# Kernel tuning notes

Measured on AMD Instinct MI355X. Metric: run time of the kernel, lower is better.

## Reference

```python
import jax, jax.numpy as jnp
import numpy as np

N_NODES = 100000
N_EDGES = 1600000
IN_C, HID_C, OUT_C = 128, 256, 128


def setup_inputs() -> dict:
    key = jax.random.key(0)
    ks = jax.random.split(key, 6)
    x = jax.random.normal(ks[0], (N_NODES, IN_C), dtype=jnp.float32)
    edge_index = jax.random.randint(ks[1], (2, N_EDGES), 0, N_NODES, dtype=jnp.int64)
    s = 0.05
    W1a = jax.random.normal(ks[2], (IN_C, HID_C), dtype=jnp.float32) * s
    b1a = jnp.zeros((HID_C,), dtype=jnp.float32)
    W2a = jax.random.normal(ks[3], (HID_C, HID_C), dtype=jnp.float32) * s
    b2a = jnp.zeros((HID_C,), dtype=jnp.float32)
    W1b = jax.random.normal(ks[4], (HID_C, HID_C), dtype=jnp.float32) * s
    b1b = jnp.zeros((HID_C,), dtype=jnp.float32)
    W2b = jax.random.normal(ks[5], (HID_C, OUT_C), dtype=jnp.float32) * s
    b2b = jnp.zeros((OUT_C,), dtype=jnp.float32)
    return {"x": x, "edge_index": edge_index, "W1a": W1a, "b1a": b1a,
            "W2a": W2a, "b2a": b2a, "W1b": W1b, "b1b": b1b,
            "W2b": W2b, "b2b": b2b}


def _gin_conv(x, src, dst, W1, b1, W2, b2):
    # GINConv (eps=0): nn( x + sum_{j in N(i)} x_j )
    agg = jax.ops.segment_sum(x[src], dst, num_segments=N_NODES)  # [N, d]
    h = x + agg
    h = jnp.maximum(h @ W1 + b1, 0.0)
    return h @ W2 + b2


def reference(x, edge_index, W1a, b1a, W2a, b2a, W1b, b1b, W2b, b2b):
    src, dst = edge_index[0], edge_index[1]
    h = jnp.maximum(_gin_conv(x, src, dst, W1a, b1a, W2a, b2a), 0.0)  # relu(conv1)
    # dropout is identity in eval mode
    out = _gin_conv(h, src, dst, W1b, b1b, W2b, b2b)  # conv2
    return out
```

## Files before the change

### kernel.cpp

```cpp
#include <hip/hip_runtime.h>


#define N_NODES 100000
#define N_EDGES 1600000
#define NBUCK 13

typedef unsigned short ushort_t;
typedef short bf16x8 __attribute__((ext_vector_type(8)));
typedef float floatx4 __attribute__((ext_vector_type(4)));

static __device__ __forceinline__ ushort_t f2bf(float f) {
    unsigned u = __float_as_uint(f);
    u = (u + 0x7FFFu + ((u >> 16) & 1u)) >> 16;
    return (ushort_t)u;
}
static __device__ __forceinline__ unsigned pack2bf(float lo, float hi) {
    return (unsigned)f2bf(lo) | ((unsigned)f2bf(hi) << 16);
}
static __device__ __forceinline__ void addu4(float* acc, const uint4 v) {
    const unsigned w0 = v.x, w1 = v.y, w2 = v.z, w3 = v.w;
    acc[0] += __uint_as_float(w0 << 16);
    acc[1] += __uint_as_float(w0 & 0xFFFF0000u);
    acc[2] += __uint_as_float(w1 << 16);
    acc[3] += __uint_as_float(w1 & 0xFFFF0000u);
    acc[4] += __uint_as_float(w2 << 16);
    acc[5] += __uint_as_float(w2 & 0xFFFF0000u);
    acc[6] += __uint_as_float(w3 << 16);
    acc[7] += __uint_as_float(w3 & 0xFFFF0000u);
}

#define GLOAD_LDS16(g, l)                                                     \
    __builtin_amdgcn_global_load_lds(                                         \
        (const __attribute__((address_space(1))) void*)(g),                   \
        (__attribute__((address_space(3))) void*)(l), 16, 0, 0)

#define NX8 (N_NODES * 128 / 8)
__global__ __launch_bounds__(256) void cvt_fused_kernel(
    const float* __restrict__ X, ushort_t* __restrict__ Xb,
    const float* __restrict__ W1a, const float* __restrict__ W2a,
    const float* __restrict__ W1b, const float* __restrict__ W2b,
    ushort_t* __restrict__ wt1a, ushort_t* __restrict__ wt2a,
    ushort_t* __restrict__ wt1b, ushort_t* __restrict__ wt2b) {
    int i = blockIdx.x * 256 + threadIdx.x;
    if (i < NX8) {
        const float4 a = ((const float4*)X)[2 * i];
        const float4 b = ((const float4*)X)[2 * i + 1];
        uint4 r;
        r.x = pack2bf(a.x, a.y);
        r.y = pack2bf(a.z, a.w);
        r.z = pack2bf(b.x, b.y);
        r.w = pack2bf(b.z, b.w);
        ((uint4*)Xb)[i] = r;
        return;
    }
    i -= NX8;
    if (i < 32768) {
        int k = i >> 8, n = i & 255;
        wt1a[n * 128 + k] = f2bf(W1a[i]);
    } else if (i < 98304) {
        int j = i - 32768, k = j >> 8, n = j & 255;
        wt2a[n * 256 + k] = f2bf(W2a[j]);
    } else if (i < 163840) {
        int j = i - 98304, k = j >> 8, n = j & 255;
        wt1b[n * 256 + k] = f2bf(W1b[j]);
    } else if (i < 196608) {
        int j = i - 163840, k = j >> 7, n = j & 127;
        wt2b[n * 256 + k] = f2bf(W2b[j]);
    }
}

__global__ __launch_bounds__(256) void hist_kernel(const int* __restrict__ src,
                                                   const int* __restrict__ dst,
                                                   int* __restrict__ deg, int nE) {
    for (int e = blockIdx.x * 256 + threadIdx.x; e < nE; e += gridDim.x * 256) {
        int d = dst[e];
        int s = src[e];
        if ((unsigned)d < (unsigned)N_NODES && (unsigned)s < (unsigned)N_NODES)
            atomicAdd(&deg[d], 1);
    }
}

__global__ __launch_bounds__(256) void fill_kernel(const int* __restrict__ src,
                                                   const int* __restrict__ dst,
                                                   int* __restrict__ cursor,
                                                   int* __restrict__ csr_src, int nE) {
    const int bucket = blockIdx.y;
    for (int e = blockIdx.x * 256 + threadIdx.x; e < nE; e += gridDim.x * 256) {
        int d = dst[e];
        int s = src[e];
        if ((unsigned)d < (unsigned)N_NODES && (unsigned)s < (unsigned)N_NODES &&
            (d >> 13) == bucket) {
            int pos = atomicAdd(&cursor[d], 1);
            csr_src[pos] = s;
        }
    }
}

__global__ __launch_bounds__(256) void scan1_kernel(const int* __restrict__ deg,
                                                    int* __restrict__ bsum, int n) {
    __shared__ int l[256];
    int b = blockIdx.x, t = threadIdx.x;
    int base = b * 1024 + t * 4;
    int s = 0;
#pragma unroll
    for (int k = 0; k < 4; ++k) {
        int i = base + k;
        if (i < n) s += deg[i];
    }
    l[t] = s;
    __syncthreads();
    for (int off = 128; off > 0; off >>= 1) {
        if (t < off) l[t] += l[t + off];
        __syncthreads();
    }
    if (t == 0) bsum[b] = l[0];
}

__global__ __launch_bounds__(128) void scan2_kernel(const int* __restrict__ bsum,
                                                    int* __restrict__ boff, int nb) {
    __shared__ int l[128];
    int t = threadIdx.x;
    int v = (t < nb) ? bsum[t] : 0;
    l[t] = v;
    __syncthreads();
    for (int off = 1; off < 128; off <<= 1) {
        int add = (t >= off) ? l[t - off] : 0;
        __syncthreads();
        l[t] += add;
        __syncthreads();
    }
    if (t < nb) boff[t] = l[t] - v;
}

__global__ __launch_bounds__(256) void scan3_kernel(const int* __restrict__ deg,
                                                    const int* __restrict__ boff,
                                                    int* __restrict__ row_ptr,
                                                    int* __restrict__ cursor, int n) {
    __shared__ int l[256];
    int b = blockIdx.x, t = threadIdx.x;
    int base = b * 1024 + t * 4;
    int d[4];
    int s = 0;
#pragma unroll
    for (int k = 0; k < 4; ++k) {
        int i = base + k;
        d[k] = (i < n) ? deg[i] : 0;
        s += d[k];
    }
    l[t] = s;
    __syncthreads();
    for (int off = 1; off < 256; off <<= 1) {
        int add = (t >= off) ? l[t - off] : 0;
        __syncthreads();
        l[t] += add;
        __syncthreads();
    }
    int run = boff[b] + l[t] - s;
#pragma unroll
    for (int k = 0; k < 4; ++k) {
        int i = base + k;
        if (i < n) {
            row_ptr[i] = run;
            cursor[i] = run;
        }
        run += d[k];
    }
}

template <int C, int U>
__global__ __launch_bounds__(256) void agg_gather_kernel(
    const ushort_t* __restrict__ X, ushort_t* __restrict__ T,
    const int* __restrict__ row_ptr, const int* __restrict__ deg,
    const int* __restrict__ csr_src, const ushort_t* __restrict__ zrow, int nN) {
    constexpr int G = C / 8;
    constexpr int NPW = 64 / G;
    constexpr int B = U * NPW;
    const int lane = threadIdx.x & 63;
    const int wid = threadIdx.x >> 6;
    const int node = blockIdx.x * 4 + wid;
    if (node >= nN) return;
    const int sub = lane / G;
    const int coff = (lane % G) * 8;

    float acc[8];
#pragma unroll
    for (int k = 0; k < 8; ++k) acc[k] = 0.f;

    const int base = row_ptr[node];
    const int dg = deg[node];
    for (int j0 = 0; j0 < dg; j0 += 64) {
        int cnt = dg - j0;
        if (cnt > 64) cnt = 64;
        int nidx = (lane < cnt) ? csr_src[base + j0 + lane] : 0;
        if ((unsigned)nidx >= (unsigned)N_NODES) nidx = 0;
        for (int j = 0; j < cnt; j += B) {
            uint4 v[U];
#pragma unroll
            for (int u = 0; u < U; ++u) {
                int jj = j + u * NPW + sub;
                bool ok = jj < cnt;
                int idx = __shfl(nidx, ok ? jj : 0);
                const ushort_t* p = ok ? (X + (size_t)idx * C) : zrow;
                v[u] = *(const uint4*)(p + coff);
            }
#pragma unroll
            for (int u = 0; u < U; ++u) addu4(acc, v[u]);
        }
    }
    if (sub == 0) {
        uint4 v = *(const uint4*)(X + (size_t)node * C + coff);
        addu4(acc, v);
    }
#pragma unroll
    for (int off = G; off < 64; off <<= 1)
#pragma unroll
        for (int k = 0; k < 8; ++k) acc[k] += __shfl_xor(acc[k], off);

    if (lane < G) {
        uint4 r;
        r.x = pack2bf(acc[0], acc[1]);
        r.y = pack2bf(acc[2], acc[3]);
        r.z = pack2bf(acc[4], acc[5]);
        r.w = pack2bf(acc[6], acc[7]);
        *(uint4*)(T + (size_t)node * C + coff) = r;
    }
}

template <int K1, int N2, bool RELU2, typename OT>
__global__ __launch_bounds__(256, 3) void mlp_kernel(
    const ushort_t* __restrict__ A, const ushort_t* __restrict__ Wt1,
    const float* __restrict__ b1, const ushort_t* __restrict__ Wt2,
    const float* __restrict__ b2, OT* __restrict__ C, int M) {
    constexpr int N1 = 256, BM = 64, BK = 32;
    constexpr int NPW2 = N2 / 4;
    constexpr int RN2 = NPW2 / 16;
    __shared__ ushort_t As[BM * BK];
    __shared__ ushort_t Bs[N1 * BK];
    __shared__ ushort_t U[BM * N1];

    const int lane = threadIdx.x & 63;
    const int wid = threadIdx.x >> 6;
    const int l15 = lane & 15;
    const int q = lane >> 4;
    const int srow = lane >> 2;
    const int scol = (lane & 3) * 8;
    const int bm = blockIdx.x * BM;

    floatx4 acc[4][4];
#pragma unroll
    for (int mi = 0; mi < 4; ++mi)
#pragma unroll
        for (int ni = 0; ni < 4; ++ni) {
            floatx4 z = {0.f, 0.f, 0.f, 0.f};
            acc[mi][ni] = z;
        }

    for (int kt = 0; kt < K1; kt += BK) {
        {
            const int gr = bm + wid * 16 + srow;
            if (gr < M)
                GLOAD_LDS16(A + (size_t)gr * K1 + kt + scol, &As[(wid * 16) * BK]);
        }
#pragma unroll
        for (int u = 0; u < 4; ++u) {
            const int row = wid * 64 + u * 16;
            GLOAD_LDS16(Wt1 + (size_t)(row + srow) * K1 + kt + scol, &Bs[row * BK]);
        }
        __syncthreads();
        bf16x8 av[4], bv[4];
#pragma unroll
        for (int mi = 0; mi < 4; ++mi)
            av[mi] = *(const bf16x8*)&Bs[(wid * 64 + mi * 16 + l15) * BK + q * 8];
#pragma unroll
        for (int ni = 0; ni < 4; ++ni)
            bv[ni] = *(const bf16x8*)&As[(ni * 16 + l15) * BK + q * 8];
#pragma unroll
        for (int mi = 0; mi < 4; ++mi)
#pragma unroll
            for (int ni = 0; ni < 4; ++ni)
                acc[mi][ni] = __builtin_amdgcn_mfma_f32_16x16x32_bf16(
                    av[mi], bv[ni], acc[mi][ni], 0, 0, 0);
        __syncthreads();
    }

#pragma unroll
    for (int mi = 0; mi < 4; ++mi) {
        const int h0 = wid * 64 + mi * 16 + q * 4;
        const float4 b4 = *(const float4*)&b1[h0];
#pragma unroll
        for (int ni = 0; ni < 4; ++ni) {
            const int node = ni * 16 + l15;
            float v0 = acc[mi][ni][0] + b4.x; v0 = v0 > 0.f ? v0 : 0.f;
            float v1 = acc[mi][ni][1] + b4.y; v1 = v1 > 0.f ? v1 : 0.f;
            float v2 = acc[mi][ni][2] + b4.z; v2 = v2 > 0.f ? v2 : 0.f;
            float v3 = acc[mi][ni][3] + b4.w; v3 = v3 > 0.f ? v3 : 0.f;
            uint2 w;
            w.x = pack2bf(v0, v1);
            w.y = pack2bf(v2, v3);
            int byte = node * (N1 * 2) + h0 * 2;
            byte ^= (node & 7) << 4;
            *(uint2*)((char*)U + byte) = w;
        }
    }
    __syncthreads();

#pragma unroll
    for (int mi = 0; mi < 4; ++mi)
#pragma unroll
        for (int ni = 0; ni < 4; ++ni) {
            floatx4 z = {0.f, 0.f, 0.f, 0.f};
            acc[mi][ni] = z;
        }

    for (int kt = 0; kt < N1; kt += BK) {
#pragma unroll
        for (int u = 0; u < RN2; ++u) {
            const int row = wid * NPW2 + u * 16;
            GLOAD_LDS16(Wt2 + (size_t)(row + srow) * N1 + kt + scol, &Bs[row * BK]);
        }
        __syncthreads();
        bf16x8 av[4], bv[RN2];
#pragma unroll
        for (int mi = 0; mi < 4; ++mi) {
            const int node = mi * 16 + l15;
            const int byte =
                (node * (N1 * 2) + kt * 2 + q * 16) ^ ((node & 7) << 4);
            av[mi] = *(const bf16x8*)((const char*)U + byte);
        }
#pragma unroll
        for (int ni = 0; ni < RN2; ++ni)
            bv[ni] = *(const bf16x8*)&Bs[(wid * NPW2 + ni * 16 + l15) * BK + q * 8];
#pragma unroll
        for (int mi = 0; mi < 4; ++mi)
#pragma unroll
            for (int ni = 0; ni < RN2; ++ni)
                acc[mi][ni] = __builtin_amdgcn_mfma_f32_16x16x32_bf16(
                    av[mi], bv[ni], acc[mi][ni], 0, 0, 0);
        __syncthreads();
    }

    float bval[RN2];
#pragma unroll
    for (int ni = 0; ni < RN2; ++ni) bval[ni] = b2[wid * NPW2 + ni * 16 + l15];
#pragma unroll
    for (int mi = 0; mi < 4; ++mi) {
#pragma unroll
        for (int r = 0; r < 4; ++r) {
            const int row = bm + mi * 16 + q * 4 + r;
            if (row < M) {
#pragma unroll
                for (int ni = 0; ni < RN2; ++ni) {
                    const int col = wid * NPW2 + ni * 16 + l15;
                    float v = acc[mi][ni][r] + bval[ni];
                    if (RELU2) v = v > 0.f ? v : 0.f;
                    if constexpr (sizeof(OT) == 2)
                        C[(size_t)row * N2 + col] = f2bf(v);
                    else
                        C[(size_t)row * N2 + col] = v;
                }
            }
        }
    }
}

extern "C" void kernel_launch(void* const* d_in, const int* in_sizes, int n_in,
                              void* d_out, int out_size, void* d_ws, size_t ws_size,
                              hipStream_t stream) {
    const float* x   = (const float*)d_in[0];
    const int*   ei  = (const int*)d_in[1];
    const float* W1a = (const float*)d_in[2];
    const float* b1a = (const float*)d_in[3];
    const float* W2a = (const float*)d_in[4];
    const float* b2a = (const float*)d_in[5];
    const float* W1b = (const float*)d_in[6];
    const float* b1b = (const float*)d_in[7];
    const float* W2b = (const float*)d_in[8];
    const float* b2b = (const float*)d_in[9];
    const int* src = ei;
    const int* dst = ei + N_EDGES;
    float* out = (float*)d_out;

    char* base = (char*)d_ws;
    size_t o = 0;
    ushort_t* wt1a = (ushort_t*)(base + o); o += 128 * 256 * 2;
    ushort_t* wt2a = (ushort_t*)(base + o); o += 256 * 256 * 2;
    ushort_t* wt1b = (ushort_t*)(base + o); o += 256 * 256 * 2;
    ushort_t* wt2b = (ushort_t*)(base + o); o += 256 * 128 * 2;
    o = (o + 255) & ~(size_t)255;
    ushort_t* zrow = (ushort_t*)(base + o); o += 512;
    int* deg     = (int*)(base + o); o += (size_t)N_NODES * 4;
    int* row_ptr = (int*)(base + o); o += (size_t)N_NODES * 4;
    int* cursor  = (int*)(base + o); o += (size_t)N_NODES * 4;
    int* bsum    = (int*)(base + o); o += 128 * 4;
    int* boff    = (int*)(base + o); o += 128 * 4;
    o = (o + 255) & ~(size_t)255;
    int* csr_src = (int*)(base + o); o += (size_t)N_EDGES * 4;
    o = (o + 255) & ~(size_t)255;
    ushort_t* t1   = (ushort_t*)(base + o); o += (size_t)N_NODES * 128 * 2;
    ushort_t* tbig = (ushort_t*)(base + o); o += (size_t)N_NODES * 256 * 2;
    o += 128 * 1024;
    (void)ws_size; (void)o; (void)in_sizes; (void)n_in; (void)out_size;

    ushort_t* inter = (ushort_t*)d_out;
    ushort_t* xb    = (ushort_t*)d_out;

    cvt_fused_kernel<<<(NX8 + 196608 + 255) / 256, 256, 0, stream>>>(
        x, xb, W1a, W2a, W1b, W2b, wt1a, wt2a, wt1b, wt2b);

    const int NB = (N_NODES + 1023) / 1024;
    hipMemsetAsync(zrow, 0, 512 + (size_t)N_NODES * 4, stream);
    hist_kernel<<<2048, 256, 0, stream>>>(src, dst, deg, N_EDGES);
    scan1_kernel<<<NB, 256, 0, stream>>>(deg, bsum, N_NODES);
    scan2_kernel<<<1, 128, 0, stream>>>(bsum, boff, NB);
    scan3_kernel<<<NB, 256, 0, stream>>>(deg, boff, row_ptr, cursor, N_NODES);
    fill_kernel<<<dim3(1024, NBUCK), 256, 0, stream>>>(src, dst, cursor, csr_src,
                                                       N_EDGES);

    const int ga = (N_NODES + 3) / 4;
    const int gf = (N_NODES + 63) / 64;

    agg_gather_kernel<128, 4><<<ga, 256, 0, stream>>>(xb, t1, row_ptr, deg,
                                                      csr_src, zrow, N_NODES);
    mlp_kernel<128, 256, true, ushort_t><<<gf, 256, 0, stream>>>(
        t1, wt1a, b1a, wt2a, b2a, inter, N_NODES);

    agg_gather_kernel<256, 8><<<ga, 256, 0, stream>>>(inter, tbig, row_ptr,
                                                      deg, csr_src, zrow, N_NODES);
    mlp_kernel<256, 128, false, float><<<gf, 256, 0, stream>>>(
        tbig, wt1b, b1b, wt2b, b2b, out, N_NODES);
}
```

Baseline: 532.4 us.

## Double-buffer LDS tiles in fused MLP kernel to overlap loads with MFMA

Splits the As and Bs shared tiles in the fused two-layer MLP kernel into two buffers each. The next K-tile's global-to-LDS load is issued before the MFMAs on the current tile, removing one barrier per iteration. The first second-layer weight tile is also prefetched while the first-layer epilogue writes the hidden activations. The larger LDS footprint forces launch bounds down from 3 to 2 blocks per CU, trading occupancy for load/compute overlap.

```diff
diff --git a/kernel.cpp b/kernel.cpp
--- a/kernel.cpp
+++ b/kernel.cpp
@@ -227,15 +227,17 @@
 }
 
 template <int K1, int N2, bool RELU2, typename OT>
-__global__ __launch_bounds__(256, 3) void mlp_kernel(
+__global__ __launch_bounds__(256, 2) void mlp_kernel(
     const ushort_t* __restrict__ A, const ushort_t* __restrict__ Wt1,
     const float* __restrict__ b1, const ushort_t* __restrict__ Wt2,
     const float* __restrict__ b2, OT* __restrict__ C, int M) {
     constexpr int N1 = 256, BM = 64, BK = 32;
     constexpr int NPW2 = N2 / 4;
     constexpr int RN2 = NPW2 / 16;
-    __shared__ ushort_t As[BM * BK];
-    __shared__ ushort_t Bs[N1 * BK];
+    constexpr int NT1 = K1 / BK;
+    constexpr int NT2 = N1 / BK;
+    __shared__ ushort_t As[2][BM * BK];
+    __shared__ ushort_t Bs[2][N1 * BK];
     __shared__ ushort_t U[BM * N1];
 
     const int lane = threadIdx.x & 63;
@@ -246,6 +248,26 @@
     const int scol = (lane & 3) * 8;
     const int bm = blockIdx.x * BM;
 
+    auto stage1 = [&](int bf, int kt) {
+        const int gr = bm + wid * 16 + srow;
+        if (gr < M)
+            GLOAD_LDS16(A + (size_t)gr * K1 + kt + scol, &As[bf][(wid * 16) * BK]);
+#pragma unroll
+        for (int u = 0; u < 4; ++u) {
+            const int row = wid * 64 + u * 16;
+            GLOAD_LDS16(Wt1 + (size_t)(row + srow) * K1 + kt + scol,
+                        &Bs[bf][row * BK]);
+        }
+    };
+    auto stage2 = [&](int bf, int kt) {
+#pragma unroll
+        for (int u = 0; u < RN2; ++u) {
+            const int row = wid * NPW2 + u * 16;
+            GLOAD_LDS16(Wt2 + (size_t)(row + srow) * N1 + kt + scol,
+                        &Bs[bf][row * BK]);
+        }
+    };
+
     floatx4 acc[4][4];
 #pragma unroll
     for (int mi = 0; mi < 4; ++mi)
@@ -255,25 +277,18 @@
             acc[mi][ni] = z;
         }
 
-    for (int kt = 0; kt < K1; kt += BK) {
-        {
-            const int gr = bm + wid * 16 + srow;
-            if (gr < M)
-                GLOAD_LDS16(A + (size_t)gr * K1 + kt + scol, &As[(wid * 16) * BK]);
-        }
-#pragma unroll
-        for (int u = 0; u < 4; ++u) {
-            const int row = wid * 64 + u * 16;
-            GLOAD_LDS16(Wt1 + (size_t)(row + srow) * K1 + kt + scol, &Bs[row * BK]);
-        }
-        __syncthreads();
+    stage1(0, 0);
+    __syncthreads();
+    for (int t = 0; t < NT1; ++t) {
+        if (t + 1 < NT1) stage1((t + 1) & 1, (t + 1) * BK);
+        const int cb = t & 1;
         bf16x8 av[4], bv[4];
 #pragma unroll
         for (int mi = 0; mi < 4; ++mi)
-            av[mi] = *(const bf16x8*)&Bs[(wid * 64 + mi * 16 + l15) * BK + q * 8];
+            av[mi] = *(const bf16x8*)&Bs[cb][(wid * 64 + mi * 16 + l15) * BK + q * 8];
 #pragma unroll
         for (int ni = 0; ni < 4; ++ni)
-            bv[ni] = *(const bf16x8*)&As[(ni * 16 + l15) * BK + q * 8];
+            bv[ni] = *(const bf16x8*)&As[cb][(ni * 16 + l15) * BK + q * 8];
 #pragma unroll
         for (int mi = 0; mi < 4; ++mi)
 #pragma unroll
@@ -282,6 +297,8 @@
                     av[mi], bv[ni], acc[mi][ni], 0, 0, 0);
         __syncthreads();
     }
+
+    stage2(0, 0);
 
 #pragma unroll
     for (int mi = 0; mi < 4; ++mi) {
@@ -312,13 +329,10 @@
             acc[mi][ni] = z;
         }
 
-    for (int kt = 0; kt < N1; kt += BK) {
-#pragma unroll
-        for (int u = 0; u < RN2; ++u) {
-            const int row = wid * NPW2 + u * 16;
-            GLOAD_LDS16(Wt2 + (size_t)(row + srow) * N1 + kt + scol, &Bs[row * BK]);
-        }
-        __syncthreads();
+    for (int t = 0; t < NT2; ++t) {
+        if (t + 1 < NT2) stage2((t + 1) & 1, (t + 1) * BK);
+        const int cb = t & 1;
+        const int kt = t * BK;
         bf16x8 av[4], bv[RN2];
 #pragma unroll
         for (int mi = 0; mi < 4; ++mi) {
@@ -329,7 +343,7 @@
         }
 #pragma unroll
         for (int ni = 0; ni < RN2; ++ni)
-            bv[ni] = *(const bf16x8*)&Bs[(wid * NPW2 + ni * 16 + l15) * BK + q * 8];
+            bv[ni] = *(const bf16x8*)&Bs[cb][(wid * NPW2 + ni * 16 + l15) * BK + q * 8];
 #pragma unroll
         for (int mi = 0; mi < 4; ++mi)
 #pragma unroll
```

Result: slower. 544.5 us (+2.3%).

## Fuse degree histogram into conversion kernel, halve fill buckets, pack accumulators

Applied to the files above, without the earlier changes.

Merges the edge degree histogram into the bf16 conversion launch as extra blocks, which removes one kernel launch and lets the two independent jobs overlap. The CSR fill pass now uses 7 destination buckets of 16384 nodes instead of 13 of 8192, so the edge list is re-read fewer times, at the cost of a larger atomic/write footprint per bucket. The gather accumulators become float2 vectors, which may let the compiler emit packed FP32 adds. The memset is moved ahead of the fused kernel so deg is zeroed before the histogram atomics run.

```diff
diff --git a/kernel.cpp b/kernel.cpp
--- a/kernel.cpp
+++ b/kernel.cpp
@@ -3,11 +3,12 @@
 
 #define N_NODES 100000
 #define N_EDGES 1600000
-#define NBUCK 13
+#define NBUCK 7
 
 typedef unsigned short ushort_t;
 typedef short bf16x8 __attribute__((ext_vector_type(8)));
 typedef float floatx4 __attribute__((ext_vector_type(4)));
+typedef float floatx2 __attribute__((ext_vector_type(2)));
 
 static __device__ __forceinline__ ushort_t f2bf(float f) {
     unsigned u = __float_as_uint(f);
@@ -17,16 +18,16 @@
 static __device__ __forceinline__ unsigned pack2bf(float lo, float hi) {
     return (unsigned)f2bf(lo) | ((unsigned)f2bf(hi) << 16);
 }
-static __device__ __forceinline__ void addu4(float* acc, const uint4 v) {
+static __device__ __forceinline__ void addu4(floatx2* acc, const uint4 v) {
     const unsigned w0 = v.x, w1 = v.y, w2 = v.z, w3 = v.w;
-    acc[0] += __uint_as_float(w0 << 16);
-    acc[1] += __uint_as_float(w0 & 0xFFFF0000u);
-    acc[2] += __uint_as_float(w1 << 16);
-    acc[3] += __uint_as_float(w1 & 0xFFFF0000u);
-    acc[4] += __uint_as_float(w2 << 16);
-    acc[5] += __uint_as_float(w2 & 0xFFFF0000u);
-    acc[6] += __uint_as_float(w3 << 16);
-    acc[7] += __uint_as_float(w3 & 0xFFFF0000u);
+    floatx2 a0 = {__uint_as_float(w0 << 16), __uint_as_float(w0 & 0xFFFF0000u)};
+    floatx2 a1 = {__uint_as_float(w1 << 16), __uint_as_float(w1 & 0xFFFF0000u)};
+    floatx2 a2 = {__uint_as_float(w2 << 16), __uint_as_float(w2 & 0xFFFF0000u)};
+    floatx2 a3 = {__uint_as_float(w3 << 16), __uint_as_float(w3 & 0xFFFF0000u)};
+    acc[0] += a0;
+    acc[1] += a1;
+    acc[2] += a2;
+    acc[3] += a3;
 }
 
 #define GLOAD_LDS16(g, l)                                                     \
@@ -35,12 +36,16 @@
         (__attribute__((address_space(3))) void*)(l), 16, 0, 0)
 
 #define NX8 (N_NODES * 128 / 8)
+#define CVT_TOTAL (NX8 + 196608)
+#define HIST_THREADS (2048 * 256)
 __global__ __launch_bounds__(256) void cvt_fused_kernel(
     const float* __restrict__ X, ushort_t* __restrict__ Xb,
     const float* __restrict__ W1a, const float* __restrict__ W2a,
     const float* __restrict__ W1b, const float* __restrict__ W2b,
     ushort_t* __restrict__ wt1a, ushort_t* __restrict__ wt2a,
-    ushort_t* __restrict__ wt1b, ushort_t* __restrict__ wt2b) {
+    ushort_t* __restrict__ wt1b, ushort_t* __restrict__ wt2b,
+    const int* __restrict__ src, const int* __restrict__ dst,
+    int* __restrict__ deg, int nE) {
     int i = blockIdx.x * 256 + threadIdx.x;
     if (i < NX8) {
         const float4 a = ((const float4*)X)[2 * i];
@@ -53,26 +58,24 @@
         ((uint4*)Xb)[i] = r;
         return;
     }
-    i -= NX8;
-    if (i < 32768) {
-        int k = i >> 8, n = i & 255;
-        wt1a[n * 128 + k] = f2bf(W1a[i]);
-    } else if (i < 98304) {
-        int j = i - 32768, k = j >> 8, n = j & 255;
-        wt2a[n * 256 + k] = f2bf(W2a[j]);
-    } else if (i < 163840) {
-        int j = i - 98304, k = j >> 8, n = j & 255;
-        wt1b[n * 256 + k] = f2bf(W1b[j]);
-    } else if (i < 196608) {
-        int j = i - 163840, k = j >> 7, n = j & 127;
-        wt2b[n * 256 + k] = f2bf(W2b[j]);
-    }
-}
-
-__global__ __launch_bounds__(256) void hist_kernel(const int* __restrict__ src,
-                                                   const int* __restrict__ dst,
-                                                   int* __restrict__ deg, int nE) {
-    for (int e = blockIdx.x * 256 + threadIdx.x; e < nE; e += gridDim.x * 256) {
+    if (i < CVT_TOTAL) {
+        i -= NX8;
+        if (i < 32768) {
+            int k = i >> 8, n = i & 255;
+            wt1a[n * 128 + k] = f2bf(W1a[i]);
+        } else if (i < 98304) {
+            int j = i - 32768, k = j >> 8, n = j & 255;
+            wt2a[n * 256 + k] = f2bf(W2a[j]);
+        } else if (i < 163840) {
+            int j = i - 98304, k = j >> 8, n = j & 255;
+            wt1b[n * 256 + k] = f2bf(W1b[j]);
+        } else {
+            int j = i - 163840, k = j >> 7, n = j & 127;
+            wt2b[n * 256 + k] = f2bf(W2b[j]);
+        }
+        return;
+    }
+    for (int e = i - CVT_TOTAL; e < nE; e += HIST_THREADS) {
         int d = dst[e];
         int s = src[e];
         if ((unsigned)d < (unsigned)N_NODES && (unsigned)s < (unsigned)N_NODES)
@@ -89,7 +92,7 @@
         int d = dst[e];
         int s = src[e];
         if ((unsigned)d < (unsigned)N_NODES && (unsigned)s < (unsigned)N_NODES &&
-            (d >> 13) == bucket) {
+            (d >> 14) == bucket) {
             int pos = atomicAdd(&cursor[d], 1);
             csr_src[pos] = s;
         }
@@ -182,9 +185,12 @@
     const int sub = lane / G;
     const int coff = (lane % G) * 8;
 
-    float acc[8];
-#pragma unroll
-    for (int k = 0; k < 8; ++k) acc[k] = 0.f;
+    floatx2 acc[4];
+#pragma unroll
+    for (int k = 0; k < 4; ++k) {
+        floatx2 z = {0.f, 0.f};
+        acc[k] = z;
+    }
 
     const int base = row_ptr[node];
     const int dg = deg[node];
@@ -214,14 +220,17 @@
 #pragma unroll
     for (int off = G; off < 64; off <<= 1)
 #pragma unroll
-        for (int k = 0; k < 8; ++k) acc[k] += __shfl_xor(acc[k], off);
+        for (int k = 0; k < 4; ++k) {
+            acc[k][0] += __shfl_xor(acc[k][0], off);
+            acc[k][1] += __shfl_xor(acc[k][1], off);
+        }
 
     if (lane < G) {
         uint4 r;
-        r.x = pack2bf(acc[0], acc[1]);
-        r.y = pack2bf(acc[2], acc[3]);
-        r.z = pack2bf(acc[4], acc[5]);
-        r.w = pack2bf(acc[6], acc[7]);
+        r.x = pack2bf(acc[0][0], acc[0][1]);
+        r.y = pack2bf(acc[1][0], acc[1][1]);
+        r.z = pack2bf(acc[2][0], acc[2][1]);
+        r.w = pack2bf(acc[3][0], acc[3][1]);
         *(uint4*)(T + (size_t)node * C + coff) = r;
     }
 }
@@ -404,12 +413,12 @@
     ushort_t* inter = (ushort_t*)d_out;
     ushort_t* xb    = (ushort_t*)d_out;
 
-    cvt_fused_kernel<<<(NX8 + 196608 + 255) / 256, 256, 0, stream>>>(
-        x, xb, W1a, W2a, W1b, W2b, wt1a, wt2a, wt1b, wt2b);
+    hipMemsetAsync(zrow, 0, 512 + (size_t)N_NODES * 4, stream);
+
+    cvt_fused_kernel<<<CVT_TOTAL / 256 + 2048, 256, 0, stream>>>(
+        x, xb, W1a, W2a, W1b, W2b, wt1a, wt2a, wt1b, wt2b, src, dst, deg, N_EDGES);
 
     const int NB = (N_NODES + 1023) / 1024;
-    hipMemsetAsync(zrow, 0, 512 + (size_t)N_NODES * 4, stream);
-    hist_kernel<<<2048, 256, 0, stream>>>(src, dst, deg, N_EDGES);
     scan1_kernel<<<NB, 256, 0, stream>>>(deg, bsum, N_NODES);
     scan2_kernel<<<1, 128, 0, stream>>>(bsum, boff, NB);
     scan3_kernel<<<NB, 256, 0, stream>>>(deg, boff, row_ptr, cursor, N_NODES);
```

Result: no change. 538.9 us (+1.2%).

## Fuse histogram into convert kernel, merge scan passes, widen MLP to 8 waves

Applied to the files above, without the earlier changes.

The degree histogram now runs inside the fused conversion kernel as extra blocks, and the separate block-offset scan kernel is removed: each scan3 block reduces the preceding block sums itself. This drops two launches. The MLP kernel moves to 512 threads (8 waves), with each wave taking half the hidden and output columns. That halves per-wave accumulator registers and aims for more waves in flight, but adds idle waves during A-tile loads and more work per barrier.

```diff
diff --git a/kernel.cpp b/kernel.cpp
--- a/kernel.cpp
+++ b/kernel.cpp
@@ -35,12 +35,16 @@
         (__attribute__((address_space(3))) void*)(l), 16, 0, 0)
 
 #define NX8 (N_NODES * 128 / 8)
+#define CVT_TOTAL (NX8 + 196608)
+#define HIST_THREADS (2048 * 256)
 __global__ __launch_bounds__(256) void cvt_fused_kernel(
     const float* __restrict__ X, ushort_t* __restrict__ Xb,
     const float* __restrict__ W1a, const float* __restrict__ W2a,
     const float* __restrict__ W1b, const float* __restrict__ W2b,
     ushort_t* __restrict__ wt1a, ushort_t* __restrict__ wt2a,
-    ushort_t* __restrict__ wt1b, ushort_t* __restrict__ wt2b) {
+    ushort_t* __restrict__ wt1b, ushort_t* __restrict__ wt2b,
+    const int* __restrict__ src, const int* __restrict__ dst,
+    int* __restrict__ deg, int nE) {
     int i = blockIdx.x * 256 + threadIdx.x;
     if (i < NX8) {
         const float4 a = ((const float4*)X)[2 * i];
@@ -53,26 +57,24 @@
         ((uint4*)Xb)[i] = r;
         return;
     }
-    i -= NX8;
-    if (i < 32768) {
-        int k = i >> 8, n = i & 255;
-        wt1a[n * 128 + k] = f2bf(W1a[i]);
-    } else if (i < 98304) {
-        int j = i - 32768, k = j >> 8, n = j & 255;
-        wt2a[n * 256 + k] = f2bf(W2a[j]);
-    } else if (i < 163840) {
-        int j = i - 98304, k = j >> 8, n = j & 255;
-        wt1b[n * 256 + k] = f2bf(W1b[j]);
-    } else if (i < 196608) {
-        int j = i - 163840, k = j >> 7, n = j & 127;
-        wt2b[n * 256 + k] = f2bf(W2b[j]);
-    }
-}
-
-__global__ __launch_bounds__(256) void hist_kernel(const int* __restrict__ src,
-                                                   const int* __restrict__ dst,
-                                                   int* __restrict__ deg, int nE) {
-    for (int e = blockIdx.x * 256 + threadIdx.x; e < nE; e += gridDim.x * 256) {
+    if (i < CVT_TOTAL) {
+        i -= NX8;
+        if (i < 32768) {
+            int k = i >> 8, n = i & 255;
+            wt1a[n * 128 + k] = f2bf(W1a[i]);
+        } else if (i < 98304) {
+            int j = i - 32768, k = j >> 8, n = j & 255;
+            wt2a[n * 256 + k] = f2bf(W2a[j]);
+        } else if (i < 163840) {
+            int j = i - 98304, k = j >> 8, n = j & 255;
+            wt1b[n * 256 + k] = f2bf(W1b[j]);
+        } else {
+            int j = i - 163840, k = j >> 7, n = j & 127;
+            wt2b[n * 256 + k] = f2bf(W2b[j]);
+        }
+        return;
+    }
+    for (int e = i - CVT_TOTAL; e < nE; e += HIST_THREADS) {
         int d = dst[e];
         int s = src[e];
         if ((unsigned)d < (unsigned)N_NODES && (unsigned)s < (unsigned)N_NODES)
@@ -116,28 +118,22 @@
     if (t == 0) bsum[b] = l[0];
 }
 
-__global__ __launch_bounds__(128) void scan2_kernel(const int* __restrict__ bsum,
-                                                    int* __restrict__ boff, int nb) {
-    __shared__ int l[128];
-    int t = threadIdx.x;
-    int v = (t < nb) ? bsum[t] : 0;
-    l[t] = v;
+__global__ __launch_bounds__(256) void scan3_kernel(const int* __restrict__ deg,
+                                                    const int* __restrict__ bsum,
+                                                    int* __restrict__ row_ptr,
+                                                    int* __restrict__ cursor,
+                                                    int n, int nb) {
+    __shared__ int l[256];
+    __shared__ int boffs;
+    int b = blockIdx.x, t = threadIdx.x;
+    l[t] = (t < b && t < nb) ? bsum[t] : 0;
     __syncthreads();
-    for (int off = 1; off < 128; off <<= 1) {
-        int add = (t >= off) ? l[t - off] : 0;
-        __syncthreads();
-        l[t] += add;
-        __syncthreads();
-    }
-    if (t < nb) boff[t] = l[t] - v;
-}
-
-__global__ __launch_bounds__(256) void scan3_kernel(const int* __restrict__ deg,
-                                                    const int* __restrict__ boff,
-                                                    int* __restrict__ row_ptr,
-                                                    int* __restrict__ cursor, int n) {
-    __shared__ int l[256];
-    int b = blockIdx.x, t = threadIdx.x;
+    for (int off = 128; off > 0; off >>= 1) {
+        if (t < off) l[t] += l[t + off];
+        __syncthreads();
+    }
+    if (t == 0) boffs = l[0];
+    __syncthreads();
     int base = b * 1024 + t * 4;
     int d[4];
     int s = 0;
@@ -155,7 +151,7 @@
         l[t] += add;
         __syncthreads();
     }
-    int run = boff[b] + l[t] - s;
+    int run = boffs + l[t] - s;
 #pragma unroll
     for (int k = 0; k < 4; ++k) {
         int i = base + k;
@@ -227,12 +223,12 @@
 }
 
 template <int K1, int N2, bool RELU2, typename OT>
-__global__ __launch_bounds__(256, 3) void mlp_kernel(
+__global__ __launch_bounds__(512, 4) void mlp_kernel(
     const ushort_t* __restrict__ A, const ushort_t* __restrict__ Wt1,
     const float* __restrict__ b1, const ushort_t* __restrict__ Wt2,
     const float* __restrict__ b2, OT* __restrict__ C, int M) {
     constexpr int N1 = 256, BM = 64, BK = 32;
-    constexpr int NPW2 = N2 / 4;
+    constexpr int NPW2 = N2 / 8;
     constexpr int RN2 = NPW2 / 16;
     __shared__ ushort_t As[BM * BK];
     __shared__ ushort_t Bs[N1 * BK];
@@ -246,54 +242,54 @@
     const int scol = (lane & 3) * 8;
     const int bm = blockIdx.x * BM;
 
-    floatx4 acc[4][4];
-#pragma unroll
-    for (int mi = 0; mi < 4; ++mi)
+    floatx4 acc1[2][4];
+#pragma unroll
+    for (int mi = 0; mi < 2; ++mi)
 #pragma unroll
         for (int ni = 0; ni < 4; ++ni) {
             floatx4 z = {0.f, 0.f, 0.f, 0.f};
-            acc[mi][ni] = z;
+            acc1[mi][ni] = z;
         }
 
     for (int kt = 0; kt < K1; kt += BK) {
-        {
+        if (wid < 4) {
             const int gr = bm + wid * 16 + srow;
             if (gr < M)
                 GLOAD_LDS16(A + (size_t)gr * K1 + kt + scol, &As[(wid * 16) * BK]);
         }
 #pragma unroll
-        for (int u = 0; u < 4; ++u) {
-            const int row = wid * 64 + u * 16;
+        for (int u = 0; u < 2; ++u) {
+            const int row = wid * 32 + u * 16;
             GLOAD_LDS16(Wt1 + (size_t)(row + srow) * K1 + kt + scol, &Bs[row * BK]);
         }
         __syncthreads();
-        bf16x8 av[4], bv[4];
-#pragma unroll
-        for (int mi = 0; mi < 4; ++mi)
-            av[mi] = *(const bf16x8*)&Bs[(wid * 64 + mi * 16 + l15) * BK + q * 8];
+        bf16x8 av[2], bv[4];
+#pragma unroll
+        for (int mi = 0; mi < 2; ++mi)
+            av[mi] = *(const bf16x8*)&Bs[(wid * 32 + mi * 16 + l15) * BK + q * 8];
 #pragma unroll
         for (int ni = 0; ni < 4; ++ni)
             bv[ni] = *(const bf16x8*)&As[(ni * 16 + l15) * BK + q * 8];
 #pragma unroll
-        for (int mi = 0; mi < 4; ++mi)
+        for (int mi = 0; mi < 2; ++mi)
 #pragma unroll
             for (int ni = 0; ni < 4; ++ni)
-                acc[mi][ni] = __builtin_amdgcn_mfma_f32_16x16x32_bf16(
-                    av[mi], bv[ni], acc[mi][ni], 0, 0, 0);
-        __syncthreads();
-    }
-
-#pragma unroll
-    for (int mi = 0; mi < 4; ++mi) {
-        const int h0 = wid * 64 + mi * 16 + q * 4;
+                acc1[mi][ni] = __builtin_amdgcn_mfma_f32_16x16x32_bf16(
+                    av[mi], bv[ni], acc1[mi][ni], 0, 0, 0);
+        __syncthreads();
+    }
+
+#pragma unroll
+    for (int mi = 0; mi < 2; ++mi) {
+        const int h0 = wid * 32 + mi * 16 + q * 4;
         const float4 b4 = *(const float4*)&b1[h0];
 #pragma unroll
         for (int ni = 0; ni < 4; ++ni) {
             const int node = ni * 16 + l15;
-            float v0 = acc[mi][ni][0] + b4.x; v0 = v0 > 0.f ? v0 : 0.f;
-            float v1 = acc[mi][ni][1] + b4.y; v1 = v1 > 0.f ? v1 : 0.f;
-            float v2 = acc[mi][ni][2] + b4.z; v2 = v2 > 0.f ? v2 : 0.f;
-            float v3 = acc[mi][ni][3] + b4.w; v3 = v3 > 0.f ? v3 : 0.f;
+            float v0 = acc1[mi][ni][0] + b4.x; v0 = v0 > 0.f ? v0 : 0.f;
+            float v1 = acc1[mi][ni][1] + b4.y; v1 = v1 > 0.f ? v1 : 0.f;
+            float v2 = acc1[mi][ni][2] + b4.z; v2 = v2 > 0.f ? v2 : 0.f;
+            float v3 = acc1[mi][ni][3] + b4.w; v3 = v3 > 0.f ? v3 : 0.f;
             uint2 w;
             w.x = pack2bf(v0, v1);
             w.y = pack2bf(v2, v3);
@@ -304,19 +300,22 @@
     }
     __syncthreads();
 
+    floatx4 acc2[4][RN2];
 #pragma unroll
     for (int mi = 0; mi < 4; ++mi)
 #pragma unroll
-        for (int ni = 0; ni < 4; ++ni) {
+        for (int ni = 0; ni < RN2; ++ni) {
             floatx4 z = {0.f, 0.f, 0.f, 0.f};
-            acc[mi][ni] = z;
+            acc2[mi][ni] = z;
         }
 
     for (int kt = 0; kt < N1; kt += BK) {
 #pragma unroll
-        for (int u = 0; u < RN2; ++u) {
-            const int row = wid * NPW2 + u * 16;
-            GLOAD_LDS16(Wt2 + (size_t)(row + srow) * N1 + kt + scol, &Bs[row * BK]);
+        for (int u = 0; u < 2; ++u) {
+            const int row = wid * 32 + u * 16;
+            if (row < N2)
+                GLOAD_LDS16(Wt2 + (size_t)(row + srow) * N1 + kt + scol,
+                            &Bs[row * BK]);
         }
         __syncthreads();
         bf16x8 av[4], bv[RN2];
@@ -334,8 +333,8 @@
         for (int mi = 0; mi < 4; ++mi)
 #pragma unroll
             for (int ni = 0; ni < RN2; ++ni)
-                acc[mi][ni] = __builtin_amdgcn_mfma_f32_16x16x32_bf16(
-                    av[mi], bv[ni], acc[mi][ni], 0, 0, 0);
+                acc2[mi][ni] = __builtin_amdgcn_mfma_f32_16x16x32_bf16(
+                    av[mi], bv[ni], acc2[mi][ni], 0, 0, 0);
         __syncthreads();
     }
 
@@ -351,7 +350,7 @@
 #pragma unroll
                 for (int ni = 0; ni < RN2; ++ni) {
                     const int col = wid * NPW2 + ni * 16 + l15;
-                    float v = acc[mi][ni][r] + bval[ni];
+                    float v = acc2[mi][ni][r] + bval[ni];
                     if (RELU2) v = v > 0.f ? v : 0.f;
                     if constexpr (sizeof(OT) == 2)
                         C[(size_t)row * N2 + col] = f2bf(v);
@@ -392,7 +391,6 @@
     int* row_ptr = (int*)(base + o); o += (size_t)N_NODES * 4;
     int* cursor  = (int*)(base + o); o += (size_t)N_NODES * 4;
     int* bsum    = (int*)(base + o); o += 128 * 4;
-    int* boff    = (int*)(base + o); o += 128 * 4;
     o = (o + 255) & ~(size_t)255;
     int* csr_src = (int*)(base + o); o += (size_t)N_EDGES * 4;
     o = (o + 255) & ~(size_t)255;
@@ -404,15 +402,14 @@
     ushort_t* inter = (ushort_t*)d_out;
     ushort_t* xb    = (ushort_t*)d_out;
 
-    cvt_fused_kernel<<<(NX8 + 196608 + 255) / 256, 256, 0, stream>>>(
-        x, xb, W1a, W2a, W1b, W2b, wt1a, wt2a, wt1b, wt2b);
+    hipMemsetAsync(zrow, 0, 512 + (size_t)N_NODES * 4, stream);
+
+    cvt_fused_kernel<<<CVT_TOTAL / 256 + 2048, 256, 0, stream>>>(
+        x, xb, W1a, W2a, W1b, W2b, wt1a, wt2a, wt1b, wt2b, src, dst, deg, N_EDGES);
 
     const int NB = (N_NODES + 1023) / 1024;
-    hipMemsetAsync(zrow, 0, 512 + (size_t)N_NODES * 4, stream);
-    hist_kernel<<<2048, 256, 0, stream>>>(src, dst, deg, N_EDGES);
     scan1_kernel<<<NB, 256, 0, stream>>>(deg, bsum, N_NODES);
-    scan2_kernel<<<1, 128, 0, stream>>>(bsum, boff, NB);
-    scan3_kernel<<<NB, 256, 0, stream>>>(deg, boff, row_ptr, cursor, N_NODES);
+    scan3_kernel<<<NB, 256, 0, stream>>>(deg, bsum, row_ptr, cursor, N_NODES, NB);
     fill_kernel<<<dim3(1024, NBUCK), 256, 0, stream>>>(src, dst, cursor, csr_src,
                                                        N_EDGES);
 
@@ -421,11 +418,11 @@
 
     agg_gather_kernel<128, 4><<<ga, 256, 0, stream>>>(xb, t1, row_ptr, deg,
                                                       csr_src, zrow, N_NODES);
-    mlp_kernel<128, 256, true, ushort_t><<<gf, 256, 0, stream>>>(
+    mlp_kernel<128, 256, true, ushort_t><<<gf, 512, 0, stream>>>(
         t1, wt1a, b1a, wt2a, b2a, inter, N_NODES);
 
     agg_gather_kernel<256, 8><<<ga, 256, 0, stream>>>(inter, tbig, row_ptr,
                                                       deg, csr_src, zrow, N_NODES);
-    mlp_kernel<256, 128, false, float><<<gf, 256, 0, stream>>>(
+    mlp_kernel<256, 128, false, float><<<gf, 512, 0, stream>>>(
         tbig, wt1b, b1b, wt2b, b2b, out, N_NODES);
 }
```

Measured after the change: 543.3 us. 1.02x slower.
